# Kernel optimization log

Hardware: AMD Instinct MI355X
Metric: run time of the kernel (lower is better)

The kernel has to match this reference:

```python
import jax, jax.numpy as jnp
import numpy as np

N = 8192        # num_node == num_hyperedges
F_DIM = 768
HID = F_DIM // 2
OUT_DIM = 10
NNZ = N * 16
DCAT = F_DIM + 2 * HID


def _lrelu(x, s):
    return jnp.where(x >= 0, x, s * x)


def _graphnorm(x, w, b, ms, eps=1e-5):
    # PyG GraphNorm, single graph: learned mean-centering then RMS over nodes
    mean = jnp.mean(x, axis=0, keepdims=True)
    out = x - ms * mean
    var = jnp.mean(out * out, axis=0, keepdims=True)
    return w * out / jnp.sqrt(var + eps) + b


def _segment_softmax(a, seg, n):
    m = jax.ops.segment_max(a, seg, num_segments=n)
    e = jnp.exp(a - m[seg])
    s = jax.ops.segment_sum(e, seg, num_segments=n)
    return e / (s[seg] + 1e-16)


def _hgconv(x, eattr, row, col, W, att, b):
    # PyG HypergraphConv, heads=1, use_attention=True, attention_mode='node'
    xt = x @ W.T          # [N, F] node lin
    et = eattr @ W.T      # [N_edges, F] hyperedge lin (shared weight)
    alpha = (xt @ att[:F_DIM])[row] + (et @ att[F_DIM:])[col]
    alpha = _lrelu(alpha, 0.2)
    alpha = _segment_softmax(alpha, col, N)  # softmax per hyperedge
    ones = jnp.ones_like(alpha)
    deg_e = jax.ops.segment_sum(ones, col, num_segments=N)
    Bn = jnp.where(deg_e > 0, 1.0 / deg_e, 0.0)
    deg_n = jax.ops.segment_sum(ones, row, num_segments=N)
    Dn = jnp.where(deg_n > 0, 1.0 / deg_n, 0.0)
    # node -> hyperedge
    efeat = jax.ops.segment_sum((Bn[col] * alpha)[:, None] * xt[row], col, num_segments=N)
    # hyperedge -> node
    out = jax.ops.segment_sum((Dn[row] * alpha)[:, None] * efeat[col], row, num_segments=N)
    return out + b


def setup_inputs() -> dict:
    key = jax.random.key(0)
    ks = jax.random.split(key, 16)
    f32 = jnp.float32
    return {
        "x": jax.random.normal(ks[0], (N, F_DIM), dtype=f32),
        "edge_index": jax.random.randint(ks[1], (2, NNZ), 0, N, dtype=jnp.int32),
        "edge_attr": jax.random.normal(ks[2], (N, F_DIM), dtype=f32),
        "gn1_w": jnp.ones((F_DIM,), f32), "gn1_b": jnp.zeros((F_DIM,), f32), "gn1_ms": jnp.ones((F_DIM,), f32),
        "gn2_w": jnp.ones((F_DIM,), f32), "gn2_b": jnp.zeros((F_DIM,), f32), "gn2_ms": jnp.ones((F_DIM,), f32),
        "hg1_W": jax.random.normal(ks[3], (F_DIM, F_DIM), dtype=f32) / np.sqrt(F_DIM),
        "hg1_att": jax.random.normal(ks[4], (2 * F_DIM,), dtype=f32) * 0.05,
        "hg1_b": jnp.zeros((F_DIM,), f32),
        "hg2_W": jax.random.normal(ks[5], (F_DIM, F_DIM), dtype=f32) / np.sqrt(F_DIM),
        "hg2_att": jax.random.normal(ks[6], (2 * F_DIM,), dtype=f32) * 0.05,
        "hg2_b": jnp.zeros((F_DIM,), f32),
        "fc1_W": jax.random.normal(ks[7], (HID, F_DIM), dtype=f32) / np.sqrt(F_DIM),
        "fc1_b": jnp.zeros((HID,), f32),
        "fc2_W": jax.random.normal(ks[8], (HID, F_DIM), dtype=f32) / np.sqrt(F_DIM),
        "fc2_b": jnp.zeros((HID,), f32),
        "attn_W1": jax.random.normal(ks[9], (N, N), dtype=f32) / np.sqrt(N),
        "attn_b1": jnp.zeros((N,), f32),
        "attn_W2": jax.random.normal(ks[10], (N,), dtype=f32) / np.sqrt(N),
        "attn_b2": jnp.zeros((), f32),
        "cls_W": jax.random.normal(ks[11], (OUT_DIM, DCAT), dtype=f32) / np.sqrt(DCAT),
        "cls_b": jnp.zeros((OUT_DIM,), f32),
        "center": jnp.zeros((DCAT,), f32),
    }


def reference(x, edge_index, edge_attr,
              gn1_w, gn1_b, gn1_ms, gn2_w, gn2_b, gn2_ms,
              hg1_W, hg1_att, hg1_b, hg2_W, hg2_att, hg2_b,
              fc1_W, fc1_b, fc2_W, fc2_b,
              attn_W1, attn_b1, attn_W2, attn_b2,
              cls_W, cls_b, center):
    row, col = edge_index[0], edge_index[1]
    h1 = _hgconv(_graphnorm(x, gn1_w, gn1_b, gn1_ms), edge_attr, row, col, hg1_W, hg1_att, hg1_b)
    h1 = _lrelu(h1, 0.01)
    out1 = _lrelu(h1 @ fc1_W.T + fc1_b, 0.01)
    h2 = _hgconv(_graphnorm(h1, gn2_w, gn2_b, gn2_ms), edge_attr, row, col, hg2_W, hg2_att, hg2_b)
    h2 = _lrelu(h2, 0.01)
    out2 = _lrelu(h2 @ fc2_W.T + fc2_b, 0.01)
    cat = jnp.concatenate([x, out1, out2], axis=1)  # [N, DCAT]
    # attention MLP over transposed features: [DCAT, N] -> [DCAT]
    score = jax.nn.relu(cat.T @ attn_W1.T + attn_b1) @ attn_W2 + attn_b2
    score = jax.nn.sigmoid(score) - center
    logits = cat * score[None, :]          # einsum 'ij,j->ij'
    return logits @ cls_W.T + cls_b        # [N, OUT_DIM]
```

## Files before the change

kernel.cpp:

```cpp
#include <hip/hip_runtime.h>
#include <cstddef>

#define NN 8192
#define FD 768
#define HIDD 384
#define NNZE 131072
#define DCATD 1536

typedef short bf16x8 __attribute__((ext_vector_type(8)));
typedef float f32x4 __attribute__((ext_vector_type(4)));

__device__ __forceinline__ short f2bf(float f){
  unsigned u = __float_as_uint(f);
  unsigned r = u + 0x7FFFu + ((u>>16)&1u);
  return (short)(r>>16);
}
__device__ __forceinline__ unsigned fmapu(float f){
  unsigned u = __float_as_uint(f);
  return (u & 0x80000000u) ? ~u : (u | 0x80000000u);
}
__device__ __forceinline__ float funmapu(unsigned m){
  unsigned u = (m & 0x80000000u) ? (m & 0x7FFFFFFFu) : ~m;
  return __uint_as_float(u);
}

__device__ __forceinline__ void async_copy16(void* lds, const void* g){
  __builtin_amdgcn_global_load_lds((__attribute__((address_space(1))) void*)g,
                                   (__attribute__((address_space(3))) void*)lds, 16, 0, 0);
}

__global__ void k_hist(const int* __restrict__ row, const int* __restrict__ col,
                       int* __restrict__ cr, int* __restrict__ cc){
  int e = blockIdx.x*256 + threadIdx.x;
  if(e >= NNZE) return;
  atomicAdd(&cc[col[e]], 1);
  atomicAdd(&cr[row[e]], 1);
}

__global__ __launch_bounds__(1024) void k_scan8192(const int* __restrict__ cnt,
                                                   int* __restrict__ offs, int* __restrict__ cur){
  __shared__ int part[1024];
  int t = threadIdx.x;
  int v[8]; int s = 0;
  #pragma unroll
  for(int j=0;j<8;j++){ v[j]=cnt[t*8+j]; s+=v[j]; }
  part[t]=s; __syncthreads();
  for(int d=1; d<1024; d<<=1){
    int mine = part[t];
    int add = (t>=d)? part[t-d] : 0;
    __syncthreads();
    part[t] = mine + add;
    __syncthreads();
  }
  int excl = part[t]-s;
  #pragma unroll
  for(int j=0;j<8;j++){ offs[t*8+j]=excl; cur[t*8+j]=excl; excl+=v[j]; }
  if(t==1023) offs[8192]=excl;
}

__global__ void k_scatter(const int* __restrict__ row, const int* __restrict__ col,
                          int* __restrict__ ccur, int* __restrict__ rcur,
                          int* __restrict__ ceids, int* __restrict__ reids){
  int e = blockIdx.x*256 + threadIdx.x;
  if(e >= NNZE) return;
  int p = atomicAdd(&ccur[col[e]],1); ceids[p]=e;
  int q = atomicAdd(&rcur[row[e]],1); reids[q]=e;
}

__global__ void k_deg(const int* __restrict__ cc, const int* __restrict__ cr,
                      float* __restrict__ Bn, float* __restrict__ Dn){
  int i = blockIdx.x*256 + threadIdx.x;
  if(i>=NN) return;
  int c=cc[i]; Bn[i] = c>0 ? 1.f/(float)c : 0.f;
  int r=cr[i]; Dn[i] = r>0 ? 1.f/(float)r : 0.f;
}

__global__ __launch_bounds__(256) void k_colstats(const float* __restrict__ src,
                                                  float* __restrict__ gs, float* __restrict__ gss){
  int col = blockIdx.x*256 + threadIdx.x;
  int r0 = blockIdx.y*256;
  float s1=0.f, s2=0.f;
  for(int r=0;r<256;r++){
    float v = src[(size_t)(r0+r)*FD + col];
    s1+=v; s2+=v*v;
  }
  atomicAdd(&gs[col], s1);
  atomicAdd(&gss[col], s2);
}

__global__ void k_gn_fin(const float* __restrict__ gs, const float* __restrict__ gss,
                         const float* __restrict__ w_, const float* __restrict__ b_,
                         const float* __restrict__ ms_, float* __restrict__ A, float* __restrict__ B){
  int c = blockIdx.x*256 + threadIdx.x;
  if(c>=FD) return;
  float mean = gs[c]*(1.f/(float)NN);
  float ex2  = gss[c]*(1.f/(float)NN);
  float ctr  = ms_[c]*mean;
  float var  = ex2 - 2.f*ctr*mean + ctr*ctr;
  float a    = w_[c] / sqrtf(var + 1e-5f);
  A[c]=a; B[c]=b_[c] - a*ctr;
}

__global__ void k_cast_bf16(const float* __restrict__ s, short* __restrict__ d, int n){
  int i = blockIdx.x*256+threadIdx.x;
  if(i<n) d[i]=f2bf(s[i]);
}
__global__ void k_affcast(const float* __restrict__ s, const float* __restrict__ A,
                          const float* __restrict__ B, short* __restrict__ d){
  int i = blockIdx.x*256+threadIdx.x;
  if(i>=NN*FD) return;
  int c = i - (i/FD)*FD;
  d[i] = f2bf(A[c]*s[i] + B[c]);
}

__global__ __launch_bounds__(256) void k_cvt8(const float* __restrict__ s, short* __restrict__ d){
  size_t base = ((size_t)blockIdx.x*256 + threadIdx.x)*8;
  float4 f0 = *(const float4*)(s+base);
  float4 f1 = *(const float4*)(s+base+4);
  bf16x8 t;
  t[0]=f2bf(f0.x); t[1]=f2bf(f0.y); t[2]=f2bf(f0.z); t[3]=f2bf(f0.w);
  t[4]=f2bf(f1.x); t[5]=f2bf(f1.y); t[6]=f2bf(f1.z); t[7]=f2bf(f1.w);
  *(bf16x8*)(d+base) = t;
}

__global__ __launch_bounds__(256) void gemm_lds(const short* __restrict__ A, const short* __restrict__ B,
    float* __restrict__ C, int M, int N, int K,
    const float* __restrict__ bias, float slope){
  __shared__ __align__(16) short As[128*32];
  __shared__ __align__(16) short Bs[128*32];
  int t = threadIdx.x;
  int w = t>>6, l = t&63;
  int m0 = blockIdx.y*128, n0 = blockIdx.x*128;
  int wm = w>>1, wn = w&1;
  int li = l&15, q = l>>4;
  const short* Ag = A + (size_t)(m0 + w*16 + (l>>2))*K + (l&3)*8;
  const short* Bg = B + (size_t)(n0 + w*16 + (l>>2))*K + (l&3)*8;
  short* Asl = &As[(w*16)*32];
  short* Bsl = &Bs[(w*16)*32];
  f32x4 acc[4][4];
  #pragma unroll
  for(int i=0;i<4;i++)
    #pragma unroll
    for(int j=0;j<4;j++) acc[i][j] = (f32x4){0.f,0.f,0.f,0.f};
  for(int k0=0;k0<K;k0+=32){
    async_copy16(Asl,          Ag + k0);
    async_copy16(Asl + 64*32,  Ag + (size_t)64*K + k0);
    async_copy16(Bsl,          Bg + k0);
    async_copy16(Bsl + 64*32,  Bg + (size_t)64*K + k0);
    __syncthreads();
    bf16x8 a[4], b[4];
    #pragma unroll
    for(int i=0;i<4;i++) a[i] = *(const bf16x8*)&As[(wm*64 + i*16 + li)*32 + q*8];
    #pragma unroll
    for(int j=0;j<4;j++) b[j] = *(const bf16x8*)&Bs[(wn*64 + j*16 + li)*32 + q*8];
    #pragma unroll
    for(int i=0;i<4;i++)
      #pragma unroll
      for(int j=0;j<4;j++)
        acc[i][j] = __builtin_amdgcn_mfma_f32_16x16x32_bf16(a[i], b[j], acc[i][j], 0, 0, 0);
    __syncthreads();
  }
  #pragma unroll
  for(int i=0;i<4;i++){
    int gm = m0 + wm*64 + i*16 + q*4;
    #pragma unroll
    for(int j=0;j<4;j++){
      int gn = n0 + wn*64 + j*16 + li;
      float bv = bias ? bias[gn] : 0.f;
      #pragma unroll
      for(int r=0;r<4;r++){
        float vv = acc[i][j][r] + bv;
        vv = (vv>=0.f) ? vv : vv*slope;
        C[(size_t)(gm+r)*N + gn] = vv;
      }
    }
  }
}

__global__ __launch_bounds__(256) void k_watt(const float* __restrict__ W, const float* __restrict__ att,
    const float* __restrict__ gnA, const float* __restrict__ gnB,
    float* __restrict__ wx, float* __restrict__ we, float* __restrict__ aconst){
  int c = blockIdx.x; int t = threadIdx.x;
  float sA=0.f, sB=0.f;
  for(int f=t; f<FD; f+=256){
    float w = W[(size_t)f*FD + c];
    sA += w*att[f];
    sB += w*att[FD+f];
  }
  __shared__ float shA[256], shB[256];
  shA[t]=sA; shB[t]=sB; __syncthreads();
  for(int s=128;s>0;s>>=1){ if(t<s){ shA[t]+=shA[t+s]; shB[t]+=shB[t+s]; } __syncthreads(); }
  if(t==0){ float a=shA[0]; wx[c]=gnA[c]*a; we[c]=shB[0]; atomicAdd(aconst, gnB[c]*a); }
}

__global__ __launch_bounds__(64) void k_matvec(const float* __restrict__ src, const float* __restrict__ wv,
    const float* __restrict__ cst, float* __restrict__ out){
  int i = blockIdx.x, l = threadIdx.x;
  float s=0.f;
  for(int c=l;c<FD;c+=64) s += src[(size_t)i*FD+c]*wv[c];
  for(int o=32;o;o>>=1) s += __shfl_down(s,o);
  if(l==0) out[i] = s + (cst ? cst[0] : 0.f);
}

__global__ void k_alpha1(const int* __restrict__ row, const int* __restrict__ col,
                         const float* __restrict__ ax, const float* __restrict__ ae,
                         float* __restrict__ araw, unsigned* __restrict__ segmax){
  int e = blockIdx.x*256 + threadIdx.x;
  if(e>=NNZE) return;
  float a = ax[row[e]] + ae[col[e]];
  a = (a>=0.f) ? a : 0.2f*a;
  araw[e]=a;
  atomicMax(&segmax[col[e]], fmapu(a));
}
__global__ void k_alpha2(const int* __restrict__ col, const float* __restrict__ araw,
                         const unsigned* __restrict__ segmax,
                         float* __restrict__ eexp, float* __restrict__ esum){
  int e = blockIdx.x*256 + threadIdx.x;
  if(e>=NNZE) return;
  float m = funmapu(segmax[col[e]]);
  float x = expf(araw[e]-m);
  eexp[e]=x;
  atomicAdd(&esum[col[e]], x);
}
__global__ void k_alpha3(const int* __restrict__ col, const float* __restrict__ eexp,
                         const float* __restrict__ esum, float* __restrict__ asm_){
  int e = blockIdx.x*256 + threadIdx.x;
  if(e>=NNZE) return;
  asm_[e] = eexp[e] / (esum[col[e]] + 1e-16f);
}

__global__ __launch_bounds__(256) void k_seg_gather(const float* __restrict__ src,
    const int* __restrict__ offs, const int* __restrict__ eids,
    const int* __restrict__ gidx, const float* __restrict__ alpha_sm,
    const float* __restrict__ segscale, const float* __restrict__ bias, float slope,
    float* __restrict__ dst){
  int c = blockIdx.x, t = threadIdx.x;
  int beg = offs[c], end = offs[c+1];
  float scale = segscale[c];
  __shared__ float wsh[256]; __shared__ int rsh[256];
  float a0=0.f,a1=0.f,a2=0.f;
  for(int base=beg; base<end; base+=256){
    int idx = base+t;
    if(idx<end){ int e=eids[idx]; wsh[t]=alpha_sm[e]; rsh[t]=gidx[e]; }
    __syncthreads();
    int cnt = min(256, end-base);
    for(int j=0;j<cnt;j++){
      float wj = wsh[j];
      const float* r = src + (size_t)rsh[j]*FD;
      a0 += wj*r[t]; a1 += wj*r[t+256]; a2 += wj*r[t+512];
    }
    __syncthreads();
  }
  a0*=scale; a1*=scale; a2*=scale;
  if(bias){
    a0+=bias[t]; a1+=bias[t+256]; a2+=bias[t+512];
    a0=(a0>=0.f)?a0:slope*a0; a1=(a1>=0.f)?a1:slope*a1; a2=(a2>=0.f)?a2:slope*a2;
  }
  dst[(size_t)c*FD+t]=a0; dst[(size_t)c*FD+t+256]=a1; dst[(size_t)c*FD+t+512]=a2;
}

__global__ __launch_bounds__(256) void k_build_catT(const float* __restrict__ x,
    const float* __restrict__ o1, const float* __restrict__ o2, short* __restrict__ catT){
  __shared__ float tile[32][33];
  int i0 = blockIdx.x*32, d0 = blockIdx.y*32;
  int tx = threadIdx.x, ty = threadIdx.y;
  const float* src; int dof, ld;
  if(d0 < FD){ src=x; dof=d0; ld=FD; }
  else if(d0 < FD+HIDD){ src=o1; dof=d0-FD; ld=HIDD; }
  else { src=o2; dof=d0-FD-HIDD; ld=HIDD; }
  for(int yy=ty; yy<32; yy+=8)
    tile[yy][tx] = src[(size_t)(i0+yy)*ld + dof + tx];
  __syncthreads();
  for(int yy=ty; yy<32; yy+=8)
    catT[(size_t)(d0+yy)*NN + i0 + tx] = f2bf(tile[tx][yy]);
}

__global__ __launch_bounds__(256) void attn_gemm_lds(const short* __restrict__ catT,
    const short* __restrict__ W1b, const float* __restrict__ b1, const float* __restrict__ W2,
    float* __restrict__ score_pre){
  const int K = NN;
  __shared__ __align__(16) short As[128*32];
  __shared__ __align__(16) short Bs[128*32];
  int id = blockIdx.x;
  int cc = id&7, g = id>>3;
  int m_idx = g%12;
  int n_idx = (g/12)*8 + cc;
  int m0 = m_idx*128, n0 = n_idx*128;
  int t = threadIdx.x;
  int w = t>>6, l = t&63;
  int wm = w>>1, wn = w&1;
  int li = l&15, q = l>>4;
  const short* Ag = catT + (size_t)(m0 + w*16 + (l>>2))*K + (l&3)*8;
  const short* Bg = W1b + (size_t)(n0 + w*16 + (l>>2))*K + (l&3)*8;
  short* Asl = &As[(w*16)*32];
  short* Bsl = &Bs[(w*16)*32];
  f32x4 acc[4][4];
  #pragma unroll
  for(int i=0;i<4;i++)
    #pragma unroll
    for(int j=0;j<4;j++) acc[i][j] = (f32x4){0.f,0.f,0.f,0.f};
  for(int k0=0;k0<K;k0+=32){
    async_copy16(Asl,          Ag + k0);
    async_copy16(Asl + 64*32,  Ag + (size_t)64*K + k0);
    async_copy16(Bsl,          Bg + k0);
    async_copy16(Bsl + 64*32,  Bg + (size_t)64*K + k0);
    __syncthreads();
    bf16x8 a[4], b[4];
    #pragma unroll
    for(int i=0;i<4;i++) a[i] = *(const bf16x8*)&As[(wm*64 + i*16 + li)*32 + q*8];
    #pragma unroll
    for(int j=0;j<4;j++) b[j] = *(const bf16x8*)&Bs[(wn*64 + j*16 + li)*32 + q*8];
    #pragma unroll
    for(int i=0;i<4;i++)
      #pragma unroll
      for(int j=0;j<4;j++)
        acc[i][j] = __builtin_amdgcn_mfma_f32_16x16x32_bf16(a[i], b[j], acc[i][j], 0, 0, 0);
    __syncthreads();
  }
  float w2v[4], b1v[4];
  #pragma unroll
  for(int j=0;j<4;j++){ int gn = n0 + wn*64 + j*16 + li; w2v[j]=W2[gn]; b1v[j]=b1[gn]; }
  #pragma unroll
  for(int i=0;i<4;i++){
    #pragma unroll
    for(int r=0;r<4;r++){
      float s=0.f;
      #pragma unroll
      for(int j=0;j<4;j++){
        float v = acc[i][j][r] + b1v[j];
        v = v>0.f ? v : 0.f;
        s += v*w2v[j];
      }
      s += __shfl_xor(s,1); s += __shfl_xor(s,2); s += __shfl_xor(s,4); s += __shfl_xor(s,8);
      if(li==0) atomicAdd(&score_pre[m0 + wm*64 + i*16 + q*4 + r], s);
    }
  }
}

__global__ __launch_bounds__(256) void attn_gemm_f32(const short* __restrict__ catT,
    const float* __restrict__ W1, const float* __restrict__ b1, const float* __restrict__ W2,
    float* __restrict__ score_pre){
  const int K = NN;
  int lane = threadIdx.x & 63;
  int wv   = threadIdx.x >> 6;
  int m0 = (blockIdx.x*4 + wv)*64;
  int n0 = blockIdx.y*64;
  int li = lane & 15, q = lane >> 4;
  const short* Ab = catT + (size_t)(m0+li)*K + q*8;
  const float* Bb = W1 + (size_t)(n0+li)*K + q*8;
  f32x4 acc[4][4];
  #pragma unroll
  for(int i=0;i<4;i++)
    #pragma unroll
    for(int j=0;j<4;j++) acc[i][j] = (f32x4){0.f,0.f,0.f,0.f};
  for(int k0=0;k0<K;k0+=32){
    bf16x8 a[4], b[4];
    #pragma unroll
    for(int i=0;i<4;i++) a[i] = *(const bf16x8*)(Ab + (size_t)i*16*K + k0);
    #pragma unroll
    for(int j=0;j<4;j++){
      const float* p = Bb + (size_t)j*16*K + k0;
      float4 f0 = *(const float4*)p;
      float4 f1 = *(const float4*)(p+4);
      bf16x8 t;
      t[0]=f2bf(f0.x); t[1]=f2bf(f0.y); t[2]=f2bf(f0.z); t[3]=f2bf(f0.w);
      t[4]=f2bf(f1.x); t[5]=f2bf(f1.y); t[6]=f2bf(f1.z); t[7]=f2bf(f1.w);
      b[j]=t;
    }
    #pragma unroll
    for(int i=0;i<4;i++)
      #pragma unroll
      for(int j=0;j<4;j++)
        acc[i][j] = __builtin_amdgcn_mfma_f32_16x16x32_bf16(a[i], b[j], acc[i][j], 0, 0, 0);
  }
  float w2v[4], b1v[4];
  #pragma unroll
  for(int j=0;j<4;j++){ int gn=n0+j*16+li; w2v[j]=W2[gn]; b1v[j]=b1[gn]; }
  #pragma unroll
  for(int i=0;i<4;i++){
    #pragma unroll
    for(int r=0;r<4;r++){
      float s=0.f;
      #pragma unroll
      for(int j=0;j<4;j++){
        float v = acc[i][j][r] + b1v[j];
        v = v>0.f ? v : 0.f;
        s += v*w2v[j];
      }
      s += __shfl_xor(s,1); s += __shfl_xor(s,2); s += __shfl_xor(s,4); s += __shfl_xor(s,8);
      if(li==0) atomicAdd(&score_pre[m0 + i*16 + q*4 + r], s);
    }
  }
}

__global__ void k_score(const float* __restrict__ pre, const float* __restrict__ b2,
                        const float* __restrict__ center, const float* __restrict__ clsW,
                        float* __restrict__ sw){
  int d = blockIdx.x*256 + threadIdx.x;
  if(d>=DCATD) return;
  float sc = pre[d] + b2[0];
  sc = 1.f/(1.f+expf(-sc));
  sc -= center[d];
  #pragma unroll
  for(int o=0;o<10;o++) sw[d*10+o] = sc * clsW[(size_t)o*DCATD + d];
}

__global__ __launch_bounds__(64) void k_final(const float* __restrict__ x, const float* __restrict__ o1,
    const float* __restrict__ o2, const float* __restrict__ sw, const float* __restrict__ clsb,
    float* __restrict__ out){
  int i = blockIdx.x, l = threadIdx.x;
  float acc[10];
  #pragma unroll
  for(int o=0;o<10;o++) acc[o]=0.f;
  for(int d=l; d<DCATD; d+=64){
    float v = (d<FD) ? x[(size_t)i*FD + d]
            : (d<FD+HIDD) ? o1[(size_t)i*HIDD + d-FD]
            : o2[(size_t)i*HIDD + d-FD-HIDD];
    const float* s = sw + (size_t)d*10;
    #pragma unroll
    for(int o=0;o<10;o++) acc[o] += v*s[o];
  }
  #pragma unroll
  for(int o=0;o<10;o++){
    float t = acc[o];
    for(int off=32;off;off>>=1) t += __shfl_down(t,off);
    if(l==0) out[(size_t)i*10 + o] = t + clsb[o];
  }
}

extern "C" void kernel_launch(void* const* d_in, const int* in_sizes, int n_in,
                              void* d_out, int out_size, void* d_ws, size_t ws_size,
                              hipStream_t stream) {
  const float* x      = (const float*)d_in[0];
  const int*   ei     = (const int*)d_in[1];
  const float* eattr  = (const float*)d_in[2];
  const float* gn1_w  = (const float*)d_in[3];
  const float* gn1_b  = (const float*)d_in[4];
  const float* gn1_ms = (const float*)d_in[5];
  const float* gn2_w  = (const float*)d_in[6];
  const float* gn2_b  = (const float*)d_in[7];
  const float* gn2_ms = (const float*)d_in[8];
  const float* hg1_W  = (const float*)d_in[9];
  const float* hg1_att= (const float*)d_in[10];
  const float* hg1_b  = (const float*)d_in[11];
  const float* hg2_W  = (const float*)d_in[12];
  const float* hg2_att= (const float*)d_in[13];
  const float* hg2_b  = (const float*)d_in[14];
  const float* fc1_W  = (const float*)d_in[15];
  const float* fc1_b  = (const float*)d_in[16];
  const float* fc2_W  = (const float*)d_in[17];
  const float* fc2_b  = (const float*)d_in[18];
  const float* attn_W1= (const float*)d_in[19];
  const float* attn_b1= (const float*)d_in[20];
  const float* attn_W2= (const float*)d_in[21];
  const float* attn_b2= (const float*)d_in[22];
  const float* cls_W  = (const float*)d_in[23];
  const float* cls_b  = (const float*)d_in[24];
  const float* center = (const float*)d_in[25];
  float* out = (float*)d_out;

  const int* row = ei;
  const int* col = ei + NNZE;

  char* w = (char*)d_ws;
  size_t off = 0;
  auto alloc = [&](size_t bytes)->void*{
    off = (off + 255) & ~(size_t)255;
    void* p = w + off;
    off += bytes;
    return p;
  };
  float* xt    = (float*)alloc((size_t)NN*FD*4);
  float* ef    = (float*)alloc((size_t)NN*FD*4);
  float* h     = (float*)alloc((size_t)NN*FD*4);
  float* out1  = (float*)alloc((size_t)NN*HIDD*4);
  float* out2  = (float*)alloc((size_t)NN*HIDD*4);
  short* inb   = (short*)alloc((size_t)NN*FD*2);
  short* wb    = (short*)alloc((size_t)FD*FD*2);
  int* cnt_col = (int*)alloc(NN*4);
  int* cnt_row = (int*)alloc(NN*4);
  int* col_off = (int*)alloc((NN+1)*4);
  int* row_off = (int*)alloc((NN+1)*4);
  int* col_cur = (int*)alloc(NN*4);
  int* row_cur = (int*)alloc(NN*4);
  int* ceids   = (int*)alloc(NNZE*4);
  int* reids   = (int*)alloc(NNZE*4);
  float* Bn    = (float*)alloc(NN*4);
  float* Dn    = (float*)alloc(NN*4);
  float* a_x   = (float*)alloc(NN*4);
  float* a_e   = (float*)alloc(NN*4);
  float* araw  = (float*)alloc(NNZE*4);
  float* eexp  = (float*)alloc(NNZE*4);
  float* asm_  = (float*)alloc(NNZE*4);
  unsigned* segmax = (unsigned*)alloc(NN*4);
  float* esum  = (float*)alloc(NN*4);
  float* gsum  = (float*)alloc(FD*4);
  float* gssq  = (float*)alloc(FD*4);
  float* gnA   = (float*)alloc(FD*4);
  float* gnB   = (float*)alloc(FD*4);
  float* wx    = (float*)alloc(FD*4);
  float* we    = (float*)alloc(FD*4);
  float* aconst= (float*)alloc(256);
  float* score_pre = (float*)alloc(DCATD*4);
  float* sw    = (float*)alloc(DCATD*10*4);
  short* catT  = (short*)ef;
  size_t off_before_w1b = off;
  short* W1b   = (short*)alloc((size_t)NN*NN*2);
  bool use_w1b = (off <= ws_size);
  if(!use_w1b) off = off_before_w1b;
  (void)n_in; (void)in_sizes; (void)out_size;

  hipMemsetAsync(cnt_col, 0, NN*4, stream);
  hipMemsetAsync(cnt_row, 0, NN*4, stream);
  k_hist<<<NNZE/256, 256, 0, stream>>>(row, col, cnt_row, cnt_col);
  k_scan8192<<<1, 1024, 0, stream>>>(cnt_col, col_off, col_cur);
  k_scan8192<<<1, 1024, 0, stream>>>(cnt_row, row_off, row_cur);
  k_scatter<<<NNZE/256, 256, 0, stream>>>(row, col, col_cur, row_cur, ceids, reids);
  k_deg<<<NN/256, 256, 0, stream>>>(cnt_col, cnt_row, Bn, Dn);

  if(use_w1b)
    k_cvt8<<<(NN*(size_t)NN)/8/256, 256, 0, stream>>>(attn_W1, W1b);

  for(int layer=0; layer<2; layer++){
    const float* src_feat = (layer==0) ? x : h;
    const float* gW   = (layer==0) ? gn1_w  : gn2_w;
    const float* gB   = (layer==0) ? gn1_b  : gn2_b;
    const float* gMS  = (layer==0) ? gn1_ms : gn2_ms;
    const float* hgW  = (layer==0) ? hg1_W  : hg2_W;
    const float* hgAtt= (layer==0) ? hg1_att: hg2_att;
    const float* hgB  = (layer==0) ? hg1_b  : hg2_b;
    const float* fcW  = (layer==0) ? fc1_W  : fc2_W;
    const float* fcB  = (layer==0) ? fc1_b  : fc2_b;
    float* fout       = (layer==0) ? out1   : out2;

    hipMemsetAsync(gsum, 0, FD*4, stream);
    hipMemsetAsync(gssq, 0, FD*4, stream);
    k_colstats<<<dim3(3,32), 256, 0, stream>>>(src_feat, gsum, gssq);
    k_gn_fin<<<3, 256, 0, stream>>>(gsum, gssq, gW, gB, gMS, gnA, gnB);

    hipMemsetAsync(aconst, 0, 4, stream);
    k_watt<<<FD, 256, 0, stream>>>(hgW, hgAtt, gnA, gnB, wx, we, aconst);
    k_matvec<<<NN, 64, 0, stream>>>(src_feat, wx, aconst, a_x);
    k_matvec<<<NN, 64, 0, stream>>>(eattr, we, nullptr, a_e);

    k_affcast<<<(NN*FD)/256, 256, 0, stream>>>(src_feat, gnA, gnB, inb);
    k_cast_bf16<<<(FD*FD)/256, 256, 0, stream>>>(hgW, wb, FD*FD);
    gemm_lds<<<dim3(FD/128, NN/128), 256, 0, stream>>>(inb, wb, xt, NN, FD, FD, nullptr, 1.f);

    hipMemsetAsync(segmax, 0, NN*4, stream);
    hipMemsetAsync(esum, 0, NN*4, stream);
    k_alpha1<<<NNZE/256, 256, 0, stream>>>(row, col, a_x, a_e, araw, segmax);
    k_alpha2<<<NNZE/256, 256, 0, stream>>>(col, araw, segmax, eexp, esum);
    k_alpha3<<<NNZE/256, 256, 0, stream>>>(col, eexp, esum, asm_);

    k_seg_gather<<<NN, 256, 0, stream>>>(xt, col_off, ceids, row, asm_, Bn, nullptr, 1.f, ef);
    k_seg_gather<<<NN, 256, 0, stream>>>(ef, row_off, reids, col, asm_, Dn, hgB, 0.01f, h);

    k_cast_bf16<<<(NN*FD)/256, 256, 0, stream>>>(h, inb, NN*FD);
    k_cast_bf16<<<(HIDD*FD)/256, 256, 0, stream>>>(fcW, wb, HIDD*FD);
    gemm_lds<<<dim3(HIDD/128, NN/128), 256, 0, stream>>>(inb, wb, fout, NN, HIDD, FD, fcB, 0.01f);
  }

  k_build_catT<<<dim3(NN/32, DCATD/32), dim3(32,8), 0, stream>>>(x, out1, out2, catT);
  hipMemsetAsync(score_pre, 0, DCATD*4, stream);
  if(use_w1b)
    attn_gemm_lds<<<768, 256, 0, stream>>>(catT, W1b, attn_b1, attn_W2, score_pre);
  else
    attn_gemm_f32<<<dim3(DCATD/256, NN/64), 256, 0, stream>>>(catT, attn_W1, attn_b1, attn_W2, score_pre);
  k_score<<<DCATD/256, 256, 0, stream>>>(score_pre, attn_b2, center, cls_W, sw);
  k_final<<<NN, 64, 0, stream>>>(x, out1, out2, sw, cls_b, out);
}
```

Before: 1.330 ms.

## Fuse preprocessing, softmax, casts and gather epilogues to cut kernel launches

Several small kernels are merged into larger ones. The two scans now run as one launch and also compute the reciprocal degrees. All weight casts go into one conversion kernel. GraphNorm finalisation moves into k_watt, the affine cast is fused with the a_x dot product, and the three atomic-based softmax passes become one per-segment wave-level softmax. The gather kernel uses float4 loads with 192 threads and also writes the bf16 copy of h for the fc GEMM. The aim is fewer launches, fewer memsets, fewer intermediate buffers and less global traffic, at the cost of more complex kernels and redundant exp evaluation in the softmax.

```diff
diff --git a/kernel.cpp b/kernel.cpp
--- a/kernel.cpp
+++ b/kernel.cpp
@@ -14,14 +14,6 @@
   unsigned u = __float_as_uint(f);
   unsigned r = u + 0x7FFFu + ((u>>16)&1u);
   return (short)(r>>16);
-}
-__device__ __forceinline__ unsigned fmapu(float f){
-  unsigned u = __float_as_uint(f);
-  return (u & 0x80000000u) ? ~u : (u | 0x80000000u);
-}
-__device__ __forceinline__ float funmapu(unsigned m){
-  unsigned u = (m & 0x80000000u) ? (m & 0x7FFFFFFFu) : ~m;
-  return __uint_as_float(u);
 }
 
 __device__ __forceinline__ void async_copy16(void* lds, const void* g){
@@ -37,8 +29,15 @@
   atomicAdd(&cr[row[e]], 1);
 }
 
-__global__ __launch_bounds__(1024) void k_scan8192(const int* __restrict__ cnt,
-                                                   int* __restrict__ offs, int* __restrict__ cur){
+__global__ __launch_bounds__(1024) void k_scan2(const int* __restrict__ cnt_col,
+    const int* __restrict__ cnt_row,
+    int* __restrict__ col_off, int* __restrict__ row_off,
+    int* __restrict__ col_cur, int* __restrict__ row_cur,
+    float* __restrict__ Bn, float* __restrict__ Dn){
+  const int* cnt = (blockIdx.x==0) ? cnt_col : cnt_row;
+  int* offs = (blockIdx.x==0) ? col_off : row_off;
+  int* cur  = (blockIdx.x==0) ? col_cur : row_cur;
+  float* rec= (blockIdx.x==0) ? Bn : Dn;
   __shared__ int part[1024];
   int t = threadIdx.x;
   int v[8]; int s = 0;
@@ -54,7 +53,10 @@
   }
   int excl = part[t]-s;
   #pragma unroll
-  for(int j=0;j<8;j++){ offs[t*8+j]=excl; cur[t*8+j]=excl; excl+=v[j]; }
+  for(int j=0;j<8;j++){
+    offs[t*8+j]=excl; cur[t*8+j]=excl; excl+=v[j];
+    rec[t*8+j] = (v[j]>0) ? 1.f/(float)v[j] : 0.f;
+  }
   if(t==1023) offs[8192]=excl;
 }
 
@@ -67,12 +69,29 @@
   int q = atomicAdd(&rcur[row[e]],1); reids[q]=e;
 }
 
-__global__ void k_deg(const int* __restrict__ cc, const int* __restrict__ cr,
-                      float* __restrict__ Bn, float* __restrict__ Dn){
-  int i = blockIdx.x*256 + threadIdx.x;
-  if(i>=NN) return;
-  int c=cc[i]; Bn[i] = c>0 ? 1.f/(float)c : 0.f;
-  int r=cr[i]; Dn[i] = r>0 ? 1.f/(float)r : 0.f;
+__global__ __launch_bounds__(256) void k_cvt_all(int nW1,
+    const float* __restrict__ W1, short* __restrict__ W1b,
+    const float* __restrict__ hg1W, short* __restrict__ wb1,
+    const float* __restrict__ hg2W, short* __restrict__ wb2,
+    const float* __restrict__ fc1W, short* __restrict__ fwb1,
+    const float* __restrict__ fc2W, short* __restrict__ fwb2){
+  int b = blockIdx.x;
+  const float* s; short* d; size_t base;
+  if(b < nW1){ s=W1; d=W1b; base=(size_t)b*2048; }
+  else {
+    int r = b - nW1;
+    if(r<288){ s=hg1W; d=wb1; base=(size_t)r*2048; }
+    else if(r<576){ s=hg2W; d=wb2; base=(size_t)(r-288)*2048; }
+    else if(r<720){ s=fc1W; d=fwb1; base=(size_t)(r-576)*2048; }
+    else { s=fc2W; d=fwb2; base=(size_t)(r-720)*2048; }
+  }
+  size_t i = base + (size_t)threadIdx.x*8;
+  float4 f0 = *(const float4*)(s+i);
+  float4 f1 = *(const float4*)(s+i+4);
+  bf16x8 t;
+  t[0]=f2bf(f0.x); t[1]=f2bf(f0.y); t[2]=f2bf(f0.z); t[3]=f2bf(f0.w);
+  t[4]=f2bf(f1.x); t[5]=f2bf(f1.y); t[6]=f2bf(f1.z); t[7]=f2bf(f1.w);
+  *(bf16x8*)(d+i) = t;
 }
 
 __global__ __launch_bounds__(256) void k_colstats(const float* __restrict__ src,
@@ -88,39 +107,57 @@
   atomicAdd(&gss[col], s2);
 }
 
-__global__ void k_gn_fin(const float* __restrict__ gs, const float* __restrict__ gss,
-                         const float* __restrict__ w_, const float* __restrict__ b_,
-                         const float* __restrict__ ms_, float* __restrict__ A, float* __restrict__ B){
-  int c = blockIdx.x*256 + threadIdx.x;
-  if(c>=FD) return;
-  float mean = gs[c]*(1.f/(float)NN);
-  float ex2  = gss[c]*(1.f/(float)NN);
-  float ctr  = ms_[c]*mean;
-  float var  = ex2 - 2.f*ctr*mean + ctr*ctr;
-  float a    = w_[c] / sqrtf(var + 1e-5f);
-  A[c]=a; B[c]=b_[c] - a*ctr;
-}
-
-__global__ void k_cast_bf16(const float* __restrict__ s, short* __restrict__ d, int n){
-  int i = blockIdx.x*256+threadIdx.x;
-  if(i<n) d[i]=f2bf(s[i]);
-}
-__global__ void k_affcast(const float* __restrict__ s, const float* __restrict__ A,
-                          const float* __restrict__ B, short* __restrict__ d){
-  int i = blockIdx.x*256+threadIdx.x;
-  if(i>=NN*FD) return;
-  int c = i - (i/FD)*FD;
-  d[i] = f2bf(A[c]*s[i] + B[c]);
-}
-
-__global__ __launch_bounds__(256) void k_cvt8(const float* __restrict__ s, short* __restrict__ d){
-  size_t base = ((size_t)blockIdx.x*256 + threadIdx.x)*8;
-  float4 f0 = *(const float4*)(s+base);
-  float4 f1 = *(const float4*)(s+base+4);
-  bf16x8 t;
-  t[0]=f2bf(f0.x); t[1]=f2bf(f0.y); t[2]=f2bf(f0.z); t[3]=f2bf(f0.w);
-  t[4]=f2bf(f1.x); t[5]=f2bf(f1.y); t[6]=f2bf(f1.z); t[7]=f2bf(f1.w);
-  *(bf16x8*)(d+base) = t;
+__global__ __launch_bounds__(256) void k_watt(const float* __restrict__ W, const float* __restrict__ att,
+    const float* __restrict__ gs, const float* __restrict__ gss,
+    const float* __restrict__ w_, const float* __restrict__ b_, const float* __restrict__ ms_,
+    float* __restrict__ gnA, float* __restrict__ gnB,
+    float* __restrict__ wxr, float* __restrict__ we){
+  int c = blockIdx.x; int t = threadIdx.x;
+  float sA=0.f, sB=0.f;
+  for(int f=t; f<FD; f+=256){
+    float w = W[(size_t)f*FD + c];
+    sA += w*att[f];
+    sB += w*att[FD+f];
+  }
+  __shared__ float shA[256], shB[256];
+  shA[t]=sA; shB[t]=sB; __syncthreads();
+  for(int s=128;s>0;s>>=1){ if(t<s){ shA[t]+=shA[t+s]; shB[t]+=shB[t+s]; } __syncthreads(); }
+  if(t==0){
+    float mean = gs[c]*(1.f/(float)NN);
+    float ex2  = gss[c]*(1.f/(float)NN);
+    float ctr  = ms_[c]*mean;
+    float var  = ex2 - 2.f*ctr*mean + ctr*ctr;
+    float a    = w_[c] / sqrtf(var + 1e-5f);
+    gnA[c]=a; gnB[c]=b_[c] - a*ctr;
+    wxr[c]=shA[0]; we[c]=shB[0];
+  }
+}
+
+__global__ __launch_bounds__(64) void k_matvec(const float* __restrict__ src, const float* __restrict__ wv,
+    float* __restrict__ out){
+  int i = blockIdx.x, l = threadIdx.x;
+  float s=0.f;
+  for(int c=l;c<FD;c+=64) s += src[(size_t)i*FD+c]*wv[c];
+  for(int o=32;o;o>>=1) s += __shfl_down(s,o);
+  if(l==0) out[i] = s;
+}
+
+__global__ __launch_bounds__(256) void k_affdot(const float* __restrict__ src,
+    const float* __restrict__ A, const float* __restrict__ B, const float* __restrict__ wxr,
+    short* __restrict__ dstb, float* __restrict__ ax){
+  int i = blockIdx.x, t = threadIdx.x;
+  float p = 0.f;
+  #pragma unroll
+  for(int k=0;k<3;k++){
+    int c = t + k*256;
+    float v = A[c]*src[(size_t)i*FD+c] + B[c];
+    dstb[(size_t)i*FD+c] = f2bf(v);
+    p += v*wxr[c];
+  }
+  __shared__ float sh[256];
+  sh[t]=p; __syncthreads();
+  for(int s=128;s>0;s>>=1){ if(t<s) sh[t]+=sh[t+s]; __syncthreads(); }
+  if(t==0) ax[i]=sh[0];
 }
 
 __global__ __launch_bounds__(256) void gemm_lds(const short* __restrict__ A, const short* __restrict__ B,
@@ -177,86 +214,84 @@
   }
 }
 
-__global__ __launch_bounds__(256) void k_watt(const float* __restrict__ W, const float* __restrict__ att,
-    const float* __restrict__ gnA, const float* __restrict__ gnB,
-    float* __restrict__ wx, float* __restrict__ we, float* __restrict__ aconst){
-  int c = blockIdx.x; int t = threadIdx.x;
-  float sA=0.f, sB=0.f;
-  for(int f=t; f<FD; f+=256){
-    float w = W[(size_t)f*FD + c];
-    sA += w*att[f];
-    sB += w*att[FD+f];
-  }
-  __shared__ float shA[256], shB[256];
-  shA[t]=sA; shB[t]=sB; __syncthreads();
-  for(int s=128;s>0;s>>=1){ if(t<s){ shA[t]+=shA[t+s]; shB[t]+=shB[t+s]; } __syncthreads(); }
-  if(t==0){ float a=shA[0]; wx[c]=gnA[c]*a; we[c]=shB[0]; atomicAdd(aconst, gnB[c]*a); }
-}
-
-__global__ __launch_bounds__(64) void k_matvec(const float* __restrict__ src, const float* __restrict__ wv,
-    const float* __restrict__ cst, float* __restrict__ out){
-  int i = blockIdx.x, l = threadIdx.x;
-  float s=0.f;
-  for(int c=l;c<FD;c+=64) s += src[(size_t)i*FD+c]*wv[c];
-  for(int o=32;o;o>>=1) s += __shfl_down(s,o);
-  if(l==0) out[i] = s + (cst ? cst[0] : 0.f);
-}
-
-__global__ void k_alpha1(const int* __restrict__ row, const int* __restrict__ col,
-                         const float* __restrict__ ax, const float* __restrict__ ae,
-                         float* __restrict__ araw, unsigned* __restrict__ segmax){
-  int e = blockIdx.x*256 + threadIdx.x;
-  if(e>=NNZE) return;
-  float a = ax[row[e]] + ae[col[e]];
-  a = (a>=0.f) ? a : 0.2f*a;
-  araw[e]=a;
-  atomicMax(&segmax[col[e]], fmapu(a));
-}
-__global__ void k_alpha2(const int* __restrict__ col, const float* __restrict__ araw,
-                         const unsigned* __restrict__ segmax,
-                         float* __restrict__ eexp, float* __restrict__ esum){
-  int e = blockIdx.x*256 + threadIdx.x;
-  if(e>=NNZE) return;
-  float m = funmapu(segmax[col[e]]);
-  float x = expf(araw[e]-m);
-  eexp[e]=x;
-  atomicAdd(&esum[col[e]], x);
-}
-__global__ void k_alpha3(const int* __restrict__ col, const float* __restrict__ eexp,
-                         const float* __restrict__ esum, float* __restrict__ asm_){
-  int e = blockIdx.x*256 + threadIdx.x;
-  if(e>=NNZE) return;
-  asm_[e] = eexp[e] / (esum[col[e]] + 1e-16f);
-}
-
-__global__ __launch_bounds__(256) void k_seg_gather(const float* __restrict__ src,
+__global__ __launch_bounds__(256) void k_softmax_seg(const int* __restrict__ offs,
+    const int* __restrict__ eids, const int* __restrict__ row,
+    const float* __restrict__ ax, const float* __restrict__ ae, float* __restrict__ asm_){
+  int seg = blockIdx.x*4 + (threadIdx.x>>6);
+  int l = threadIdx.x & 63;
+  int beg = offs[seg], end = offs[seg+1];
+  if(beg >= end) return;
+  float aev = ae[seg];
+  float m = -1e30f;
+  for(int idx=beg+l; idx<end; idx+=64){
+    int e = eids[idx];
+    float a = ax[row[e]] + aev; a = (a>=0.f)?a:0.2f*a;
+    m = fmaxf(m, a);
+  }
+  #pragma unroll
+  for(int o=1;o<64;o<<=1) m = fmaxf(m, __shfl_xor(m,o));
+  float s = 0.f;
+  for(int idx=beg+l; idx<end; idx+=64){
+    int e = eids[idx];
+    float a = ax[row[e]] + aev; a = (a>=0.f)?a:0.2f*a;
+    s += expf(a-m);
+  }
+  #pragma unroll
+  for(int o=1;o<64;o<<=1) s += __shfl_xor(s,o);
+  float inv = 1.f/(s + 1e-16f);
+  for(int idx=beg+l; idx<end; idx+=64){
+    int e = eids[idx];
+    float a = ax[row[e]] + aev; a = (a>=0.f)?a:0.2f*a;
+    asm_[e] = expf(a-m)*inv;
+  }
+}
+
+__global__ __launch_bounds__(192) void k_seg_gather(const float* __restrict__ src,
     const int* __restrict__ offs, const int* __restrict__ eids,
     const int* __restrict__ gidx, const float* __restrict__ alpha_sm,
     const float* __restrict__ segscale, const float* __restrict__ bias, float slope,
-    float* __restrict__ dst){
+    float* __restrict__ dst, short* __restrict__ dstb){
   int c = blockIdx.x, t = threadIdx.x;
   int beg = offs[c], end = offs[c+1];
   float scale = segscale[c];
-  __shared__ float wsh[256]; __shared__ int rsh[256];
-  float a0=0.f,a1=0.f,a2=0.f;
-  for(int base=beg; base<end; base+=256){
+  __shared__ float wsh[192]; __shared__ int rsh[192];
+  float4 acc = {0.f,0.f,0.f,0.f};
+  for(int base=beg; base<end; base+=192){
     int idx = base+t;
     if(idx<end){ int e=eids[idx]; wsh[t]=alpha_sm[e]; rsh[t]=gidx[e]; }
     __syncthreads();
-    int cnt = min(256, end-base);
-    for(int j=0;j<cnt;j++){
-      float wj = wsh[j];
-      const float* r = src + (size_t)rsh[j]*FD;
-      a0 += wj*r[t]; a1 += wj*r[t+256]; a2 += wj*r[t+512];
+    int cnt = min(192, end-base);
+    int j=0;
+    for(; j+1<cnt; j+=2){
+      float w0=wsh[j], w1=wsh[j+1];
+      float4 v0 = *((const float4*)(src + (size_t)rsh[j]*FD) + t);
+      float4 v1 = *((const float4*)(src + (size_t)rsh[j+1]*FD) + t);
+      acc.x += w0*v0.x + w1*v1.x;
+      acc.y += w0*v0.y + w1*v1.y;
+      acc.z += w0*v0.z + w1*v1.z;
+      acc.w += w0*v0.w + w1*v1.w;
     }
-    __syncthreads();
-  }
-  a0*=scale; a1*=scale; a2*=scale;
+    if(j<cnt){
+      float w0=wsh[j];
+      float4 v0 = *((const float4*)(src + (size_t)rsh[j]*FD) + t);
+      acc.x += w0*v0.x; acc.y += w0*v0.y; acc.z += w0*v0.z; acc.w += w0*v0.w;
+    }
+    __syncthreads();
+  }
+  acc.x*=scale; acc.y*=scale; acc.z*=scale; acc.w*=scale;
   if(bias){
-    a0+=bias[t]; a1+=bias[t+256]; a2+=bias[t+512];
-    a0=(a0>=0.f)?a0:slope*a0; a1=(a1>=0.f)?a1:slope*a1; a2=(a2>=0.f)?a2:slope*a2;
-  }
-  dst[(size_t)c*FD+t]=a0; dst[(size_t)c*FD+t+256]=a1; dst[(size_t)c*FD+t+512]=a2;
+    float4 bv = *((const float4*)bias + t);
+    acc.x+=bv.x; acc.y+=bv.y; acc.z+=bv.z; acc.w+=bv.w;
+    acc.x=(acc.x>=0.f)?acc.x:slope*acc.x;
+    acc.y=(acc.y>=0.f)?acc.y:slope*acc.y;
+    acc.z=(acc.z>=0.f)?acc.z:slope*acc.z;
+    acc.w=(acc.w>=0.f)?acc.w:slope*acc.w;
+  }
+  *((float4*)(dst + (size_t)c*FD) + t) = acc;
+  if(dstb){
+    short4 o; o.x=f2bf(acc.x); o.y=f2bf(acc.y); o.z=f2bf(acc.z); o.w=f2bf(acc.w);
+    *((short4*)(dstb + (size_t)c*FD) + t) = o;
+  }
 }
 
 __global__ __launch_bounds__(256) void k_build_catT(const float* __restrict__ x,
@@ -476,7 +511,11 @@
   float* out1  = (float*)alloc((size_t)NN*HIDD*4);
   float* out2  = (float*)alloc((size_t)NN*HIDD*4);
   short* inb   = (short*)alloc((size_t)NN*FD*2);
-  short* wb    = (short*)alloc((size_t)FD*FD*2);
+  short* hbf   = (short*)alloc((size_t)NN*FD*2);
+  short* wb1   = (short*)alloc((size_t)FD*FD*2);
+  short* wb2   = (short*)alloc((size_t)FD*FD*2);
+  short* fwb1  = (short*)alloc((size_t)HIDD*FD*2);
+  short* fwb2  = (short*)alloc((size_t)HIDD*FD*2);
   int* cnt_col = (int*)alloc(NN*4);
   int* cnt_row = (int*)alloc(NN*4);
   int* col_off = (int*)alloc((NN+1)*4);
@@ -489,18 +528,13 @@
   float* Dn    = (float*)alloc(NN*4);
   float* a_x   = (float*)alloc(NN*4);
   float* a_e   = (float*)alloc(NN*4);
-  float* araw  = (float*)alloc(NNZE*4);
-  float* eexp  = (float*)alloc(NNZE*4);
   float* asm_  = (float*)alloc(NNZE*4);
-  unsigned* segmax = (unsigned*)alloc(NN*4);
-  float* esum  = (float*)alloc(NN*4);
   float* gsum  = (float*)alloc(FD*4);
   float* gssq  = (float*)alloc(FD*4);
   float* gnA   = (float*)alloc(FD*4);
   float* gnB   = (float*)alloc(FD*4);
-  float* wx    = (float*)alloc(FD*4);
+  float* wxr   = (float*)alloc(FD*4);
   float* we    = (float*)alloc(FD*4);
-  float* aconst= (float*)alloc(256);
   float* score_pre = (float*)alloc(DCATD*4);
   float* sw    = (float*)alloc(DCATD*10*4);
   short* catT  = (short*)ef;
@@ -510,16 +544,14 @@
   if(!use_w1b) off = off_before_w1b;
   (void)n_in; (void)in_sizes; (void)out_size;
 
-  hipMemsetAsync(cnt_col, 0, NN*4, stream);
-  hipMemsetAsync(cnt_row, 0, NN*4, stream);
+  hipMemsetAsync(cnt_col, 0, 2*NN*4, stream);
   k_hist<<<NNZE/256, 256, 0, stream>>>(row, col, cnt_row, cnt_col);
-  k_scan8192<<<1, 1024, 0, stream>>>(cnt_col, col_off, col_cur);
-  k_scan8192<<<1, 1024, 0, stream>>>(cnt_row, row_off, row_cur);
+  k_scan2<<<2, 1024, 0, stream>>>(cnt_col, cnt_row, col_off, row_off, col_cur, row_cur, Bn, Dn);
   k_scatter<<<NNZE/256, 256, 0, stream>>>(row, col, col_cur, row_cur, ceids, reids);
-  k_deg<<<NN/256, 256, 0, stream>>>(cnt_col, cnt_row, Bn, Dn);
-
-  if(use_w1b)
-    k_cvt8<<<(NN*(size_t)NN)/8/256, 256, 0, stream>>>(attn_W1, W1b);
+
+  int nW1 = use_w1b ? (int)((size_t)NN*NN/2048) : 0;
+  k_cvt_all<<<nW1 + 864, 256, 0, stream>>>(nW1, attn_W1, W1b,
+      hg1_W, wb1, hg2_W, wb2, fc1_W, fwb1, fc2_W, fwb2);
 
   for(int layer=0; layer<2; layer++){
     const float* src_feat = (layer==0) ? x : h;
@@ -529,36 +561,21 @@
     const float* hgW  = (layer==0) ? hg1_W  : hg2_W;
     const float* hgAtt= (layer==0) ? hg1_att: hg2_att;
     const float* hgB  = (layer==0) ? hg1_b  : hg2_b;
-    const float* fcW  = (layer==0) ? fc1_W  : fc2_W;
+    const short* wbL  = (layer==0) ? wb1    : wb2;
+    const short* fwbL = (layer==0) ? fwb1   : fwb2;
     const float* fcB  = (layer==0) ? fc1_b  : fc2_b;
     float* fout       = (layer==0) ? out1   : out2;
 
-    hipMemsetAsync(gsum, 0, FD*4, stream);
-    hipMemsetAsync(gssq, 0, FD*4, stream);
+    hipMemsetAsync(gsum, 0, 2*FD*4, stream);
     k_colstats<<<dim3(3,32), 256, 0, stream>>>(src_feat, gsum, gssq);
-    k_gn_fin<<<3, 256, 0, stream>>>(gsum, gssq, gW, gB, gMS, gnA, gnB);
-
-    hipMemsetAsync(aconst, 0, 4, stream);
-    k_watt<<<FD, 256, 0, stream>>>(hgW, hgAtt, gnA, gnB, wx, we, aconst);
-    k_matvec<<<NN, 64, 0, stream>>>(src_feat, wx, aconst, a_x);
-    k_matvec<<<NN, 64, 0, stream>>>(eattr, we, nullptr, a_e);
-
-    k_affcast<<<(NN*FD)/256, 256, 0, stream>>>(src_feat, gnA, gnB, inb);
-    k_cast_bf16<<<(FD*FD)/256, 256, 0, stream>>>(hgW, wb, FD*FD);
-    gemm_lds<<<dim3(FD/128, NN/128), 256, 0, stream>>>(inb, wb, xt, NN, FD, FD, nullptr, 1.f);
-
-    hipMemsetAsync(segmax, 0, NN*4, stream);
-    hipMemsetAsync(esum, 0, NN*4, stream);
-    k_alpha1<<<NNZE/256, 256, 0, stream>>>(row, col, a_x, a_e, araw, segmax);
-    k_alpha2<<<NNZE/256, 256, 0, stream>>>(col, araw, segmax, eexp, esum);
-    k_alpha3<<<NNZE/256, 256, 0, stream>>>(col, eexp, esum, asm_);
-
-    k_seg_gather<<<NN, 256, 0, stream>>>(xt, col_off, ceids, row, asm_, Bn, nullptr, 1.f, ef);
-    k_seg_gather<<<NN, 256, 0, stream>>>(ef, row_off, reids, col, asm_, Dn, hgB, 0.01f, h);
-
-    k_cast_bf16<<<(NN*FD)/256, 256, 0, stream>>>(h, inb, NN*FD);
-    k_cast_bf16<<<(HIDD*FD)/256, 256, 0, stream>>>(fcW, wb, HIDD*FD);
-    gemm_lds<<<dim3(HIDD/128, NN/128), 256, 0, stream>>>(inb, wb, fout, NN, HIDD, FD, fcB, 0.01f);
+    k_watt<<<FD, 256, 0, stream>>>(hgW, hgAtt, gsum, gssq, gW, gB, gMS, gnA, gnB, wxr, we);
+    k_matvec<<<NN, 64, 0, stream>>>(eattr, we, a_e);
+    k_affdot<<<NN, 256, 0, stream>>>(src_feat, gnA, gnB, wxr, inb, a_x);
+    gemm_lds<<<dim3(FD/128, NN/128), 256, 0, stream>>>(inb, wbL, xt, NN, FD, FD, nullptr, 1.f);
+    k_softmax_seg<<<NN/4, 256, 0, stream>>>(col_off, ceids, row, a_x, a_e, asm_);
+    k_seg_gather<<<NN, 192, 0, stream>>>(xt, col_off, ceids, row, asm_, Bn, nullptr, 1.f, ef, nullptr);
+    k_seg_gather<<<NN, 192, 0, stream>>>(ef, row_off, reids, col, asm_, Dn, hgB, 0.01f, h, hbf);
+    gemm_lds<<<dim3(HIDD/128, NN/128), 256, 0, stream>>>(hbf, fwbL, fout, NN, HIDD, FD, fcB, 0.01f);
   }
 
   k_build_catT<<<dim3(NN/32, DCATD/32), dim3(32,8), 0, stream>>>(x, out1, out2, catT);
```

Measured after the change: 1.226 ms. -7.8%, faster.
